# Kernel tuning notes

Hardware: AMD Instinct MI355X
Metric: run time of the kernel (lower is better)

The kernel has to match this reference:

```python
import jax, jax.numpy as jnp
import numpy as np
import math

D_MODEL = 1024
N_HEADS = 16
D_K = D_MODEL // N_HEADS
B, L = 4, 2048


def setup_inputs() -> dict:
    key = jax.random.key(0)
    ks = jax.random.split(key, 11)
    s = 1.0 / math.sqrt(D_MODEL)
    inp = {
        "queries": jax.random.normal(ks[0], (B, L, D_MODEL), jnp.float32),
        "keys": jax.random.normal(ks[1], (B, L, D_MODEL), jnp.float32),
        "values": jax.random.normal(ks[2], (B, L, D_MODEL), jnp.float32),
        "Wq": jax.random.normal(ks[3], (D_MODEL, D_MODEL), jnp.float32) * s,
        "bq": jax.random.normal(ks[4], (D_MODEL,), jnp.float32) * s,
        "Wk": jax.random.normal(ks[5], (D_MODEL, D_MODEL), jnp.float32) * s,
        "bk": jax.random.normal(ks[6], (D_MODEL,), jnp.float32) * s,
        "Wv": jax.random.normal(ks[7], (D_MODEL, D_MODEL), jnp.float32) * s,
        "bv": jax.random.normal(ks[8], (D_MODEL,), jnp.float32) * s,
        "Wo": jax.random.normal(ks[9], (D_MODEL, D_MODEL), jnp.float32) * s,
        "bo": jax.random.normal(ks[10], (D_MODEL,), jnp.float32) * s,
    }
    return inp


def _heads(x):
    b, l, _ = x.shape
    return x.reshape(b, l, N_HEADS, D_K).transpose(0, 2, 1, 3)  # (B,H,L,Dk)


def reference(queries, keys, values, Wq, bq, Wk, bk, Wv, bv, Wo, bo):
    Q = _heads(queries @ Wq.T + bq)
    K = _heads(keys @ Wk.T + bk)
    V = _heads(values @ Wv.T + bv)
    scores = jnp.einsum("bhqd,bhkd->bhqk", Q, K) / math.sqrt(D_K)
    t = jnp.arange(L, dtype=scores.dtype)
    time_bias = -0.1 * jnp.abs(t[None, :] - t[:, None])  # (L,L)
    attn = jax.nn.softmax(scores + time_bias[None, None], axis=-1)
    out = jnp.einsum("bhqk,bhkd->bhqd", attn, V)
    out = out.transpose(0, 2, 1, 3).reshape(queries.shape[0], L, D_MODEL)
    return out @ Wo.T + bo
```

## Files before the change

kernel.cpp:

```cpp
#include <hip/hip_runtime.h>
#include <hip/hip_bf16.h>
#include <stdint.h>

typedef __bf16 bf16x8 __attribute__((ext_vector_type(8)));
typedef float f32x4 __attribute__((ext_vector_type(4)));

__device__ __forceinline__ uint16_t f2bf(float f){
  __bf16 h = (__bf16)f;
  return __builtin_bit_cast(uint16_t, h);
}

__device__ __forceinline__ void gld_lds16(const void* g, void* l){
  __builtin_amdgcn_global_load_lds((const __attribute__((address_space(1))) void*)g,
                                   (__attribute__((address_space(3))) void*)l, 16, 0, 0);
}

__global__ void convert2(const float* __restrict__ s1, uint16_t* __restrict__ d1, int n4_1,
                         const float* __restrict__ s2, uint16_t* __restrict__ d2, int n4_2){
  int i = blockIdx.x * blockDim.x + threadIdx.x;
  const float* s; uint16_t* d;
  if (i < n4_1) { s = s1; d = d1; }
  else { i -= n4_1; if (i >= n4_2) return; s = s2; d = d2; }
  float4 v = ((const float4*)s)[i];
  ushort4 o;
  o.x = f2bf(v.x); o.y = f2bf(v.y); o.z = f2bf(v.z); o.w = f2bf(v.w);
  ((ushort4*)d)[i] = o;
}

__launch_bounds__(256, 2)
__global__ void gemm_bt(const uint16_t* __restrict__ A, const uint16_t* __restrict__ W,
                        const float* __restrict__ bias, void* __restrict__ out, int mode,
                        float oscale)
{
  __shared__ uint16_t As[2][128 * 64];
  __shared__ uint16_t Ws[2][128 * 64];
  const int tid = threadIdx.x;
  const int wave = tid >> 6, lane = tid & 63;
  const int g = lane >> 4, li = lane & 15;
  const int m0 = blockIdx.x * 128, n0 = blockIdx.y * 128;
  const int wr = (wave >> 1) * 64, wc = (wave & 1) * 64;

  f32x4 acc[4][4];
#pragma unroll
  for (int m = 0; m < 4; m++)
#pragma unroll
    for (int n = 0; n < 4; n++) acc[m][n] = f32x4{0.f, 0.f, 0.f, 0.f};

  const uint16_t* Asrc[4];
  const uint16_t* Wsrc[4];
  int cid[4];
#pragma unroll
  for (int j = 0; j < 4; j++) {
    cid[j] = j * 256 + tid;
    int row = cid[j] >> 3, c = cid[j] & 7;
    int sc = c ^ (row & 7);
    Asrc[j] = A + (size_t)(m0 + row) * 1024 + sc * 8;
    Wsrc[j] = W + (size_t)(n0 + row) * 1024 + sc * 8;
  }

#pragma unroll
  for (int j = 0; j < 4; j++) {
    gld_lds16(Asrc[j], (char*)As[0] + cid[j] * 16);
    gld_lds16(Wsrc[j], (char*)Ws[0] + cid[j] * 16);
  }
  __syncthreads();

  for (int t = 0; t < 16; t++) {
    const int cur = t & 1;
    if (t < 15) {
      const int k1 = (t + 1) * 64;
      const int nxt = cur ^ 1;
#pragma unroll
      for (int j = 0; j < 4; j++) {
        gld_lds16(Asrc[j] + k1, (char*)As[nxt] + cid[j] * 16);
        gld_lds16(Wsrc[j] + k1, (char*)Ws[nxt] + cid[j] * 16);
      }
    }

    const char* Ab = (const char*)As[cur];
    const char* Wb = (const char*)Ws[cur];
#pragma unroll
    for (int kh = 0; kh < 2; kh++) {
      bf16x8 a[4], bfr[4];
#pragma unroll
      for (int m = 0; m < 4; m++) {
        int row = wr + m * 16 + li;
        int ch = (kh * 4 + g) ^ (row & 7);
        a[m] = *(const bf16x8*)(Ab + row * 128 + ch * 16);
      }
#pragma unroll
      for (int n = 0; n < 4; n++) {
        int row = wc + n * 16 + li;
        int ch = (kh * 4 + g) ^ (row & 7);
        bfr[n] = *(const bf16x8*)(Wb + row * 128 + ch * 16);
      }
#pragma unroll
      for (int m = 0; m < 4; m++)
#pragma unroll
        for (int n = 0; n < 4; n++)
          acc[m][n] = __builtin_amdgcn_mfma_f32_16x16x32_bf16(a[m], bfr[n], acc[m][n], 0, 0, 0);
    }
    __syncthreads();
  }

  if (mode == 0) {
    uint16_t* O = (uint16_t*)out;
#pragma unroll
    for (int n = 0; n < 4; n++) {
      int col = n0 + wc + n * 16 + li;
      float bv = bias[col];
#pragma unroll
      for (int m = 0; m < 4; m++) {
        int row = m0 + wr + m * 16 + g * 4;
#pragma unroll
        for (int r = 0; r < 4; r++)
          O[(size_t)(row + r) * 1024 + col] = f2bf((acc[m][n][r] + bv) * oscale);
      }
    }
  } else if (mode == 2) {
    uint16_t* O = (uint16_t*)out;
#pragma unroll
    for (int n = 0; n < 4; n++) {
      int col = n0 + wc + n * 16 + li;
      float bv = bias[col];
#pragma unroll
      for (int m = 0; m < 4; m++) {
        int mg = m0 + wr + m * 16 + g * 4;
        int bidx = mg >> 11;
        int l = mg & 2047;
        ushort4 pk;
        pk.x = f2bf(acc[m][n][0] + bv);
        pk.y = f2bf(acc[m][n][1] + bv);
        pk.z = f2bf(acc[m][n][2] + bv);
        pk.w = f2bf(acc[m][n][3] + bv);
        *(ushort4*)(O + ((size_t)bidx * 1024 + col) * 2048 + l) = pk;
      }
    }
  } else {
    float* O = (float*)out;
#pragma unroll
    for (int n = 0; n < 4; n++) {
      int col = n0 + wc + n * 16 + li;
      float bv = bias[col];
#pragma unroll
      for (int m = 0; m < 4; m++) {
        int row = m0 + wr + m * 16 + g * 4;
#pragma unroll
        for (int r = 0; r < 4; r++)
          O[(size_t)(row + r) * 1024 + col] = acc[m][n][r] + bv;
      }
    }
  }
}

__launch_bounds__(256, 2)
__global__ void flash_attn(const uint16_t* __restrict__ Qw, const uint16_t* __restrict__ Kw,
                           const uint16_t* __restrict__ Vt, uint16_t* __restrict__ Ow)
{
  __shared__ uint16_t Ks[64 * 64];
  __shared__ uint16_t Vs[64 * 64];
  __shared__ uint16_t Ps[4][16 * 64];

  const float C2 = 0.14426950408889635f;
  const float C3 = 20.1977305724455f;

  const int tid = threadIdx.x;
  const int wave = tid >> 6, lane = tid & 63;
  const int g = lane >> 4, li = lane & 15;
  const int q0 = blockIdx.x * 64;
  const int bh = blockIdx.y;
  const int b = bh >> 4, h = bh & 15;

  const uint16_t* Qp = Qw + (size_t)(b * 2048 + q0 + wave * 16 + li) * 1024 + h * 64 + g * 8;
  bf16x8 qf0 = *(const bf16x8*)Qp;
  bf16x8 qf1 = *(const bf16x8*)(Qp + 32);

  float l_r[4] = {0.f, 0.f, 0.f, 0.f};
  f32x4 o[4];
#pragma unroll
  for (int nd = 0; nd < 4; nd++) o[nd] = f32x4{0.f, 0.f, 0.f, 0.f};

  const int cid0 = tid, cid1 = 256 + tid;
  const int kr0 = cid0 >> 3, c0 = cid0 & 7;
  const int kr1 = cid1 >> 3, c1 = cid1 & 7;
  const int sc0 = c0 ^ (kr0 & 7), sc1 = c1 ^ (kr1 & 7);

  const uint16_t* Kb0 = Kw + (size_t)(b * 2048 + kr0) * 1024 + h * 64 + sc0 * 8;
  const uint16_t* Kb1 = Kw + (size_t)(b * 2048 + kr1) * 1024 + h * 64 + sc1 * 8;
  const uint16_t* Vb0 = Vt + (size_t)(bh * 64 + kr0) * 2048 + sc0 * 8;
  const uint16_t* Vb1 = Vt + (size_t)(bh * 64 + kr1) * 2048 + sc1 * 8;

  const int kv_lo = (q0 >= 256) ? (q0 - 256) : 0;
  const int kv_hi = (q0 + 320 <= 2048) ? (q0 + 320) : 2048;
  const int tq0 = q0 + wave * 16 + g * 4;

  for (int kv0 = kv_lo; kv0 < kv_hi; kv0 += 64) {
    gld_lds16(Kb0 + (size_t)kv0 * 1024, (char*)Ks + cid0 * 16);
    gld_lds16(Kb1 + (size_t)kv0 * 1024, (char*)Ks + cid1 * 16);
    gld_lds16(Vb0 + kv0, (char*)Vs + cid0 * 16);
    gld_lds16(Vb1 + kv0, (char*)Vs + cid1 * 16);
    __syncthreads();

    float p[4][4];
#pragma unroll
    for (int n = 0; n < 4; n++) {
      int kr = n * 16 + li;
      bf16x8 bk0 = *(const bf16x8*)((const char*)Ks + kr * 128 + ((g ^ (kr & 7)) << 4));
      bf16x8 bk1 = *(const bf16x8*)((const char*)Ks + kr * 128 + (((4 + g) ^ (kr & 7)) << 4));
      f32x4 s = f32x4{0.f, 0.f, 0.f, 0.f};
      s = __builtin_amdgcn_mfma_f32_16x16x32_bf16(qf0, bk0, s, 0, 0, 0);
      s = __builtin_amdgcn_mfma_f32_16x16x32_bf16(qf1, bk1, s, 0, 0, 0);
      float dtb = (float)(tq0 - (kv0 + n * 16 + li));
#pragma unroll
      for (int r = 0; r < 4; r++) {
        float e = exp2f((s[r] - C3) - C2 * fabsf(dtb + (float)r));
        p[n][r] = e;
        l_r[r] += e;
      }
    }

#pragma unroll
    for (int n = 0; n < 4; n++)
#pragma unroll
      for (int r = 0; r < 4; r++) {
        int prow = g * 4 + r;
        int c = n * 16 + li;
        Ps[wave][prow * 64 + ((((c >> 3) ^ (prow & 7))) << 3) + (c & 7)] = f2bf(p[n][r]);
      }

    bf16x8 pa0 = *(const bf16x8*)((const char*)Ps[wave] + li * 128 + ((g ^ (li & 7)) << 4));
    bf16x8 pa1 = *(const bf16x8*)((const char*)Ps[wave] + li * 128 + (((4 + g) ^ (li & 7)) << 4));
#pragma unroll
    for (int nd = 0; nd < 4; nd++) {
      int vr = nd * 16 + li;
      bf16x8 vb0 = *(const bf16x8*)((const char*)Vs + vr * 128 + ((g ^ (vr & 7)) << 4));
      bf16x8 vb1 = *(const bf16x8*)((const char*)Vs + vr * 128 + (((4 + g) ^ (vr & 7)) << 4));
      o[nd] = __builtin_amdgcn_mfma_f32_16x16x32_bf16(pa0, vb0, o[nd], 0, 0, 0);
      o[nd] = __builtin_amdgcn_mfma_f32_16x16x32_bf16(pa1, vb1, o[nd], 0, 0, 0);
    }
    __syncthreads();
  }

#pragma unroll
  for (int r = 0; r < 4; r++) {
    float l = l_r[r];
    l += __shfl_xor(l, 1);
    l += __shfl_xor(l, 2);
    l += __shfl_xor(l, 4);
    l += __shfl_xor(l, 8);
    float inv = 1.0f / l;
    int qg = b * 2048 + q0 + wave * 16 + g * 4 + r;
#pragma unroll
    for (int nd = 0; nd < 4; nd++)
      Ow[(size_t)qg * 1024 + h * 64 + nd * 16 + li] = f2bf(o[nd][r] * inv);
  }
}

extern "C" void kernel_launch(void* const* d_in, const int* in_sizes, int n_in,
                              void* d_out, int out_size, void* d_ws, size_t ws_size,
                              hipStream_t stream) {
  const float* q  = (const float*)d_in[0];
  const float* k  = (const float*)d_in[1];
  const float* v  = (const float*)d_in[2];
  const float* Wq = (const float*)d_in[3];
  const float* bq = (const float*)d_in[4];
  const float* Wk = (const float*)d_in[5];
  const float* bk = (const float*)d_in[6];
  const float* Wv = (const float*)d_in[7];
  const float* bv = (const float*)d_in[8];
  const float* Wo = (const float*)d_in[9];
  const float* bo = (const float*)d_in[10];

  const size_t NX = (size_t)8192 * 1024;
  const size_t NW = (size_t)1024 * 1024;

  uint16_t* Xb  = (uint16_t*)d_ws;
  uint16_t* Wb  = Xb + NX;
  uint16_t* Vtw = Wb + NW;
  uint16_t* Aws = Xb;
  uint16_t* Qws = (uint16_t*)d_out;
  uint16_t* Kws = Qws + NX;

  const int n4x = (int)(NX / 4);
  const int n4w = (int)(NW / 4);
  const int gcv = (n4x + n4w) / 256;

  dim3 ggrid(64, 8);
  const float qscale = 0.18033688011112042f;

  convert2<<<gcv, 256, 0, stream>>>(q, Xb, n4x, Wq, Wb, n4w);
  gemm_bt<<<ggrid, 256, 0, stream>>>(Xb, Wb, bq, Qws, 0, qscale);

  convert2<<<gcv, 256, 0, stream>>>(k, Xb, n4x, Wk, Wb, n4w);
  gemm_bt<<<ggrid, 256, 0, stream>>>(Xb, Wb, bk, Kws, 0, 1.0f);

  convert2<<<gcv, 256, 0, stream>>>(v, Xb, n4x, Wv, Wb, n4w);
  gemm_bt<<<ggrid, 256, 0, stream>>>(Xb, Wb, bv, Vtw, 2, 1.0f);

  flash_attn<<<dim3(32, 64), 256, 0, stream>>>(Qws, Kws, Vtw, Aws);

  convert2<<<n4w / 256, 256, 0, stream>>>(Wo, Wb, n4w, (const float*)0, (uint16_t*)0, 0);
  gemm_bt<<<ggrid, 256, 0, stream>>>(Aws, Wb, bo, d_out, 3, 1.0f);
}
```

Baseline: 310.2 us.

## Double-buffer K/V tiles in flash attention and use nontemporal loads and stores

```diff
diff --git a/kernel.cpp b/kernel.cpp
--- a/kernel.cpp
+++ b/kernel.cpp
@@ -4,6 +4,8 @@
 
 typedef __bf16 bf16x8 __attribute__((ext_vector_type(8)));
 typedef float f32x4 __attribute__((ext_vector_type(4)));
+typedef float f32x4v __attribute__((ext_vector_type(4)));
+typedef unsigned short u16x4 __attribute__((ext_vector_type(4)));
 
 __device__ __forceinline__ uint16_t f2bf(float f){
   __bf16 h = (__bf16)f;
@@ -21,10 +23,10 @@
   const float* s; uint16_t* d;
   if (i < n4_1) { s = s1; d = d1; }
   else { i -= n4_1; if (i >= n4_2) return; s = s2; d = d2; }
-  float4 v = ((const float4*)s)[i];
-  ushort4 o;
+  f32x4v v = __builtin_nontemporal_load(((const f32x4v*)s) + i);
+  u16x4 o;
   o.x = f2bf(v.x); o.y = f2bf(v.y); o.z = f2bf(v.z); o.w = f2bf(v.w);
-  ((ushort4*)d)[i] = o;
+  __builtin_nontemporal_store(o, ((u16x4*)d) + i);
 }
 
 __launch_bounds__(256, 2)
@@ -114,7 +116,8 @@
         int row = m0 + wr + m * 16 + g * 4;
 #pragma unroll
         for (int r = 0; r < 4; r++)
-          O[(size_t)(row + r) * 1024 + col] = f2bf((acc[m][n][r] + bv) * oscale);
+          __builtin_nontemporal_store(f2bf((acc[m][n][r] + bv) * oscale),
+                                      &O[(size_t)(row + r) * 1024 + col]);
       }
     }
   } else if (mode == 2) {
@@ -128,12 +131,13 @@
         int mg = m0 + wr + m * 16 + g * 4;
         int bidx = mg >> 11;
         int l = mg & 2047;
-        ushort4 pk;
+        u16x4 pk;
         pk.x = f2bf(acc[m][n][0] + bv);
         pk.y = f2bf(acc[m][n][1] + bv);
         pk.z = f2bf(acc[m][n][2] + bv);
         pk.w = f2bf(acc[m][n][3] + bv);
-        *(ushort4*)(O + ((size_t)bidx * 1024 + col) * 2048 + l) = pk;
+        __builtin_nontemporal_store(pk,
+            (u16x4*)(O + ((size_t)bidx * 1024 + col) * 2048 + l));
       }
     }
   } else {
@@ -147,7 +151,8 @@
         int row = m0 + wr + m * 16 + g * 4;
 #pragma unroll
         for (int r = 0; r < 4; r++)
-          O[(size_t)(row + r) * 1024 + col] = acc[m][n][r] + bv;
+          __builtin_nontemporal_store(acc[m][n][r] + bv,
+                                      &O[(size_t)(row + r) * 1024 + col]);
       }
     }
   }
@@ -157,8 +162,8 @@
 __global__ void flash_attn(const uint16_t* __restrict__ Qw, const uint16_t* __restrict__ Kw,
                            const uint16_t* __restrict__ Vt, uint16_t* __restrict__ Ow)
 {
-  __shared__ uint16_t Ks[64 * 64];
-  __shared__ uint16_t Vs[64 * 64];
+  __shared__ uint16_t Ks[2][64 * 64];
+  __shared__ uint16_t Vs[2][64 * 64];
   __shared__ uint16_t Ps[4][16 * 64];
 
   const float C2 = 0.14426950408889635f;
@@ -167,8 +172,8 @@
   const int tid = threadIdx.x;
   const int wave = tid >> 6, lane = tid & 63;
   const int g = lane >> 4, li = lane & 15;
-  const int q0 = blockIdx.x * 64;
-  const int bh = blockIdx.y;
+  const int bh = blockIdx.x;
+  const int q0 = blockIdx.y * 64;
   const int b = bh >> 4, h = bh & 15;
 
   const uint16_t* Qp = Qw + (size_t)(b * 2048 + q0 + wave * 16 + li) * 1024 + h * 64 + g * 8;
@@ -192,21 +197,36 @@
 
   const int kv_lo = (q0 >= 256) ? (q0 - 256) : 0;
   const int kv_hi = (q0 + 320 <= 2048) ? (q0 + 320) : 2048;
+  const int ntiles = (kv_hi - kv_lo) >> 6;
   const int tq0 = q0 + wave * 16 + g * 4;
 
-  for (int kv0 = kv_lo; kv0 < kv_hi; kv0 += 64) {
-    gld_lds16(Kb0 + (size_t)kv0 * 1024, (char*)Ks + cid0 * 16);
-    gld_lds16(Kb1 + (size_t)kv0 * 1024, (char*)Ks + cid1 * 16);
-    gld_lds16(Vb0 + kv0, (char*)Vs + cid0 * 16);
-    gld_lds16(Vb1 + kv0, (char*)Vs + cid1 * 16);
+  {
+    const int kv0 = kv_lo;
+    gld_lds16(Kb0 + (size_t)kv0 * 1024, (char*)Ks[0] + cid0 * 16);
+    gld_lds16(Kb1 + (size_t)kv0 * 1024, (char*)Ks[0] + cid1 * 16);
+    gld_lds16(Vb0 + kv0, (char*)Vs[0] + cid0 * 16);
+    gld_lds16(Vb1 + kv0, (char*)Vs[0] + cid1 * 16);
+  }
+
+  for (int it = 0; it < ntiles; ++it) {
     __syncthreads();
+    const int cur = it & 1;
+    if (it + 1 < ntiles) {
+      const int kvn = kv_lo + (it + 1) * 64;
+      const int nxt = cur ^ 1;
+      gld_lds16(Kb0 + (size_t)kvn * 1024, (char*)Ks[nxt] + cid0 * 16);
+      gld_lds16(Kb1 + (size_t)kvn * 1024, (char*)Ks[nxt] + cid1 * 16);
+      gld_lds16(Vb0 + kvn, (char*)Vs[nxt] + cid0 * 16);
+      gld_lds16(Vb1 + kvn, (char*)Vs[nxt] + cid1 * 16);
+    }
+    const int kv0 = kv_lo + it * 64;
 
     float p[4][4];
 #pragma unroll
     for (int n = 0; n < 4; n++) {
       int kr = n * 16 + li;
-      bf16x8 bk0 = *(const bf16x8*)((const char*)Ks + kr * 128 + ((g ^ (kr & 7)) << 4));
-      bf16x8 bk1 = *(const bf16x8*)((const char*)Ks + kr * 128 + (((4 + g) ^ (kr & 7)) << 4));
+      bf16x8 bk0 = *(const bf16x8*)((const char*)Ks[cur] + kr * 128 + ((g ^ (kr & 7)) << 4));
+      bf16x8 bk1 = *(const bf16x8*)((const char*)Ks[cur] + kr * 128 + (((4 + g) ^ (kr & 7)) << 4));
       f32x4 s = f32x4{0.f, 0.f, 0.f, 0.f};
       s = __builtin_amdgcn_mfma_f32_16x16x32_bf16(qf0, bk0, s, 0, 0, 0);
       s = __builtin_amdgcn_mfma_f32_16x16x32_bf16(qf1, bk1, s, 0, 0, 0);
@@ -233,12 +253,11 @@
 #pragma unroll
     for (int nd = 0; nd < 4; nd++) {
       int vr = nd * 16 + li;
-      bf16x8 vb0 = *(const bf16x8*)((const char*)Vs + vr * 128 + ((g ^ (vr & 7)) << 4));
-      bf16x8 vb1 = *(const bf16x8*)((const char*)Vs + vr * 128 + (((4 + g) ^ (vr & 7)) << 4));
+      bf16x8 vb0 = *(const bf16x8*)((const char*)Vs[cur] + vr * 128 + ((g ^ (vr & 7)) << 4));
+      bf16x8 vb1 = *(const bf16x8*)((const char*)Vs[cur] + vr * 128 + (((4 + g) ^ (vr & 7)) << 4));
       o[nd] = __builtin_amdgcn_mfma_f32_16x16x32_bf16(pa0, vb0, o[nd], 0, 0, 0);
       o[nd] = __builtin_amdgcn_mfma_f32_16x16x32_bf16(pa1, vb1, o[nd], 0, 0, 0);
     }
-    __syncthreads();
   }
 
 #pragma unroll
@@ -252,7 +271,8 @@
     int qg = b * 2048 + q0 + wave * 16 + g * 4 + r;
 #pragma unroll
     for (int nd = 0; nd < 4; nd++)
-      Ow[(size_t)qg * 1024 + h * 64 + nd * 16 + li] = f2bf(o[nd][r] * inv);
+      __builtin_nontemporal_store(f2bf(o[nd][r] * inv),
+                                  &Ow[(size_t)qg * 1024 + h * 64 + nd * 16 + li]);
   }
 }
 
@@ -297,7 +317,7 @@
   convert2<<<gcv, 256, 0, stream>>>(v, Xb, n4x, Wv, Wb, n4w);
   gemm_bt<<<ggrid, 256, 0, stream>>>(Xb, Wb, bv, Vtw, 2, 1.0f);
 
-  flash_attn<<<dim3(32, 64), 256, 0, stream>>>(Qws, Kws, Vtw, Aws);
+  flash_attn<<<dim3(64, 32), 256, 0, stream>>>(Qws, Kws, Vtw, Aws);
 
   convert2<<<n4w / 256, 256, 0, stream>>>(Wo, Wb, n4w, (const float*)0, (uint16_t*)0, 0);
   gemm_bt<<<ggrid, 256, 0, stream>>>(Aws, Wb, bo, d_out, 3, 1.0f);
```

Measured after the change: 346.3 us. +11.6%, slower.
